# Performance work log

Measured on AMD Instinct MI355X. Metric: run time of the kernel, lower is better.

Reference implementation:

```python
import jax, jax.numpy as jnp
import numpy as np

EPS = 0.5


def setup_inputs() -> dict:
    key = jax.random.key(0)
    k_x, k_e, k_w1, k_b1, k_w2, k_b2 = jax.random.split(key, 6)
    N, E = 100000, 600000
    D_IN, D_HID, D_OUT = 128, 256, 128
    x = jax.random.normal(k_x, (N, D_IN), dtype=jnp.float32)
    edge_index = jax.random.randint(k_e, (2, E), 0, N, dtype=jnp.int64)
    # nn.Linear params: weight [out, in], bias [out]; kaiming-uniform-ish init
    lim1 = 1.0 / np.sqrt(D_IN)
    W1 = jax.random.uniform(k_w1, (D_HID, D_IN), minval=-lim1, maxval=lim1, dtype=jnp.float32)
    b1 = jax.random.uniform(k_b1, (D_HID,), minval=-lim1, maxval=lim1, dtype=jnp.float32)
    lim2 = 1.0 / np.sqrt(D_HID)
    W2 = jax.random.uniform(k_w2, (D_OUT, D_HID), minval=-lim2, maxval=lim2, dtype=jnp.float32)
    b2 = jax.random.uniform(k_b2, (D_OUT,), minval=-lim2, maxval=lim2, dtype=jnp.float32)
    return {"x": x, "edge_index": edge_index, "W1": W1, "b1": b1, "W2": W2, "b2": b2}


def reference(x, edge_index, W1, b1, W2, b2):
    # gather both endpoint features per edge and sum: [E, D_IN]
    s = x[edge_index[0]] + x[edge_index[1]]
    # 2-layer MLP: Linear -> ReLU -> Linear
    h = jax.nn.relu(s @ W1.T + b1)          # [E, D_HID]
    edge_attr = h @ W2.T + b2               # [E, D_OUT]
    return EPS * edge_attr
```

## Files before the change

kernel.cpp:

```cpp
#include <hip/hip_runtime.h>
#include <hip/hip_bf16.h>

#define EDGES 600000
#define DIN 128
#define DHID 256
#define DOUT 128

#define NCHUNK 37500
#define NBLK 256
#define THREADS 768
#define NWAVES 3072
#define STRIDE NWAVES

#define W2_OFF 65536
#define B1_OFF 131072
#define B2_OFF 132096
#define LDS_BYTES 132608

typedef __attribute__((ext_vector_type(4))) float floatx4;
typedef __attribute__((ext_vector_type(4))) short shortx4;
typedef __attribute__((ext_vector_type(8))) short shortx8;

__device__ inline unsigned short f2bf_rne(float f) {
    union { float f; unsigned u; } v; v.f = f;
    unsigned r = v.u + 0x7FFFu + ((v.u >> 16) & 1u);
    return (unsigned short)(r >> 16);
}

__global__ __launch_bounds__(256) void prep_kernel(
        const float* __restrict__ W1, const float* __restrict__ W2,
        unsigned short* __restrict__ ws) {
    int j = blockIdx.x * 256 + threadIdx.x;
    if (j < 4096) {
        int lane = j & 63, fs = j >> 6;
        int ks = fs & 3, t = fs >> 2;
        int hid = t * 16 + (lane & 15), q = lane >> 4;
        const float* src = W1 + hid * DIN + ks * 32 + q * 8;
        shortx8 v;
        #pragma unroll
        for (int i = 0; i < 8; ++i) v[i] = (short)f2bf_rne(src[i]);
        *((shortx8*)ws + j) = v;
    } else if (j < 12288) {
        int j2 = j - 4096;
        int lane = j2 & 63, fs = j2 >> 6;
        int ot = fs & 7, t = fs >> 3;
        int o = ot * 16 + (lane & 15), q = lane >> 4;
        const float* src = W2 + o * DHID + t * 16 + q * 4;
        shortx4 v;
        #pragma unroll
        for (int i = 0; i < 4; ++i) v[i] = (short)f2bf_rne(src[i]);
        *((shortx4*)(ws + 32768) + j2) = v;
    }
}

#define GATHER(RAW, NA, NB) do {                                              \
    const float* pa_ = x + (size_t)(NA) * DIN + q * 8;                        \
    const float* pb_ = x + (size_t)(NB) * DIN + q * 8;                        \
    _Pragma("unroll")                                                         \
    for (int ks_ = 0; ks_ < 4; ++ks_) {                                       \
        RAW[ks_*4+0] = *(const float4*)(pa_ + ks_*32);                        \
        RAW[ks_*4+1] = *(const float4*)(pa_ + ks_*32 + 4);                    \
        RAW[ks_*4+2] = *(const float4*)(pb_ + ks_*32);                        \
        RAW[ks_*4+3] = *(const float4*)(pb_ + ks_*32 + 4);                    \
    }                                                                         \
} while (0)

__global__ __launch_bounds__(THREADS, 3) void gin_kernel(
        const float* __restrict__ x, const int* __restrict__ ei,
        const float* __restrict__ b1, const float* __restrict__ b2,
        const unsigned short* __restrict__ wsw,
        float* __restrict__ out) {
    extern __shared__ char smem[];
    const int tid = threadIdx.x;
    const int lane = tid & 63, q = lane >> 4, col = lane & 15;

    const int gw = blockIdx.x * 12 + (tid >> 6);
    int ch = gw;
    const int e0 = ch * 16 + col;
    const int na0 = ei[e0];
    const int nb0 = ei[EDGES + e0];

    {
        const float4* gsrc = (const float4*)wsw;
        for (int idx = tid; idx < 8192; idx += THREADS) {
            float4 v = gsrc[idx];
            *(float4*)(smem + (size_t)idx * 16) = v;
        }
        if (tid < 384) {
            float v = (tid < 256) ? b1[tid] : b2[tid - 256];
            *(float*)(smem + B1_OFF + tid * 4) = v;
        }
    }

    float4 raw[16];
    GATHER(raw, na0, nb0);

    int naN, nbN;
    {
        const int e1 = (ch + STRIDE) * 16 + col;
        naN = ei[e1];
        nbN = ei[EDGES + e1];
    }
    __syncthreads();

    const shortx8* w1l = (const shortx8*)smem + lane;
    const shortx4* w2l = (const shortx4*)(smem + W2_OFF) + lane;
    const floatx4* b1l = (const floatx4*)(smem + B1_OFF) + q;
    const floatx4* b2l = (const floatx4*)(smem + B2_OFF) + q;

    for (;;) {
        shortx8 sfrag[4];
        #pragma unroll
        for (int ks = 0; ks < 4; ++ks) {
            float4 u0 = raw[ks*4+0], u1 = raw[ks*4+1];
            float4 v0 = raw[ks*4+2], v1 = raw[ks*4+3];
            union { shortx8 s8; __hip_bfloat162 b[4]; } pk;
            pk.b[0] = __float22bfloat162_rn(make_float2(u0.x+v0.x, u0.y+v0.y));
            pk.b[1] = __float22bfloat162_rn(make_float2(u0.z+v0.z, u0.w+v0.w));
            pk.b[2] = __float22bfloat162_rn(make_float2(u1.x+v1.x, u1.y+v1.y));
            pk.b[3] = __float22bfloat162_rn(make_float2(u1.z+v1.z, u1.w+v1.w));
            sfrag[ks] = pk.s8;
        }

        const int chN = ch + STRIDE;
        const bool haveN = (chN < NCHUNK);
        if (haveN) {
            GATHER(raw, naN, nbN);
            const int ch2 = chN + STRIDE;
            if (ch2 < NCHUNK) {
                const int e2 = ch2 * 16 + col;
                naN = ei[e2];
                nbN = ei[EDGES + e2];
            }
        }

        floatx4 acc2[8];
        #pragma unroll
        for (int ot = 0; ot < 8; ++ot) acc2[ot] = b2l[ot*4];

        #pragma unroll 1
        for (int t = 0; t < 16; ++t) {
            shortx8 a1[4];
            #pragma unroll
            for (int ks = 0; ks < 4; ++ks) a1[ks] = w1l[(t*4+ks)*64];
            floatx4 acc1 = b1l[t*4];
            #pragma unroll
            for (int ks = 0; ks < 4; ++ks)
                acc1 = __builtin_amdgcn_mfma_f32_16x16x32_bf16(a1[ks], sfrag[ks], acc1, 0, 0, 0);
            union { shortx4 s4; __hip_bfloat162 b[2]; } pk;
            pk.b[0] = __float22bfloat162_rn(make_float2(fmaxf(acc1[0], 0.f), fmaxf(acc1[1], 0.f)));
            pk.b[1] = __float22bfloat162_rn(make_float2(fmaxf(acc1[2], 0.f), fmaxf(acc1[3], 0.f)));
            const shortx4 hf = pk.s4;
            #pragma unroll
            for (int ot = 0; ot < 8; ++ot) {
                shortx4 wb = w2l[(t*8+ot)*64];
                acc2[ot] = __builtin_amdgcn_mfma_f32_16x16x16bf16_1k(wb, hf, acc2[ot], 0, 0, 0);
            }
        }

        {
            float* op = out + (size_t)(ch * 16 + col) * DOUT + q * 4;
            #pragma unroll
            for (int ot = 0; ot < 8; ++ot) {
                floatx4 v = acc2[ot] * 0.5f;
                __builtin_nontemporal_store(v, (floatx4*)(op + ot * 16));
            }
        }

        if (!haveN) break;
        ch = chN;
    }
}

extern "C" void kernel_launch(void* const* d_in, const int* in_sizes, int n_in,
                              void* d_out, int out_size, void* d_ws, size_t ws_size,
                              hipStream_t stream) {
    const float* x  = (const float*)d_in[0];
    const int*   ei = (const int*)d_in[1];
    const float* W1 = (const float*)d_in[2];
    const float* b1 = (const float*)d_in[3];
    const float* W2 = (const float*)d_in[4];
    const float* b2 = (const float*)d_in[5];
    unsigned short* ws = (unsigned short*)d_ws;

    static bool attr_done = false;
    if (!attr_done) {
        (void)hipFuncSetAttribute((const void*)gin_kernel,
                                  hipFuncAttributeMaxDynamicSharedMemorySize,
                                  LDS_BYTES);
        attr_done = true;
    }

    prep_kernel<<<48, 256, 0, stream>>>(W1, W2, ws);
    gin_kernel<<<NBLK, THREADS, LDS_BYTES, stream>>>(x, ei, b1, b2, ws, (float*)d_out);
}
```

Before: 470.5 us.

## Pre-convert node features to bf16 to halve gather traffic

Adds a prep kernel that converts x to bf16 in workspace, and the main kernel gathers bf16 rows instead of fp32, halving gather bytes and register footprint for the prefetch buffer. Sums are computed from bf16-rounded inputs, which adds a small extra rounding before the sum. Output stores switch from nontemporal to regular stores. A fallback fp32 path is kept when the workspace is too small.

```diff
diff --git a/kernel.cpp b/kernel.cpp
--- a/kernel.cpp
+++ b/kernel.cpp
@@ -5,17 +5,20 @@
 #define DIN 128
 #define DHID 256
 #define DOUT 128
+#define NNODES 100000
 
 #define NCHUNK 37500
 #define NBLK 256
 #define THREADS 768
-#define NWAVES 3072
-#define STRIDE NWAVES
+#define STRIDE 3072
 
 #define W2_OFF 65536
 #define B1_OFF 131072
 #define B2_OFF 132096
 #define LDS_BYTES 132608
+
+#define XB_OFF_SHORTS 65536
+#define WS_BYTES_NEEDED (131072ull + (unsigned long long)NNODES * DIN * 2ull)
 
 typedef __attribute__((ext_vector_type(4))) float floatx4;
 typedef __attribute__((ext_vector_type(4))) short shortx4;
@@ -53,20 +56,22 @@
     }
 }
 
-#define GATHER(RAW, NA, NB) do {                                              \
-    const float* pa_ = x + (size_t)(NA) * DIN + q * 8;                        \
-    const float* pb_ = x + (size_t)(NB) * DIN + q * 8;                        \
-    _Pragma("unroll")                                                         \
-    for (int ks_ = 0; ks_ < 4; ++ks_) {                                       \
-        RAW[ks_*4+0] = *(const float4*)(pa_ + ks_*32);                        \
-        RAW[ks_*4+1] = *(const float4*)(pa_ + ks_*32 + 4);                    \
-        RAW[ks_*4+2] = *(const float4*)(pb_ + ks_*32);                        \
-        RAW[ks_*4+3] = *(const float4*)(pb_ + ks_*32 + 4);                    \
-    }                                                                         \
-} while (0)
-
+__global__ __launch_bounds__(256) void prep_x(
+        const float* __restrict__ x, unsigned short* __restrict__ xb) {
+    const int total = NNODES * DIN / 4;
+    for (int i = blockIdx.x * 256 + threadIdx.x; i < total; i += gridDim.x * 256) {
+        float4 v = ((const float4*)x)[i];
+        shortx4 o;
+        o[0] = (short)f2bf_rne(v.x); o[1] = (short)f2bf_rne(v.y);
+        o[2] = (short)f2bf_rne(v.z); o[3] = (short)f2bf_rne(v.w);
+        *((shortx4*)xb + i) = o;
+    }
+}
+
+template <bool BFX>
 __global__ __launch_bounds__(THREADS, 3) void gin_kernel(
-        const float* __restrict__ x, const int* __restrict__ ei,
+        const float* __restrict__ x, const unsigned short* __restrict__ xb,
+        const int* __restrict__ ei,
         const float* __restrict__ b1, const float* __restrict__ b2,
         const unsigned short* __restrict__ wsw,
         float* __restrict__ out) {
@@ -76,6 +81,32 @@
 
     const int gw = blockIdx.x * 12 + (tid >> 6);
     int ch = gw;
+
+    float4  rawf[BFX ? 1 : 16];
+    shortx8 rawb[BFX ? 8 : 1];
+
+    auto gather = [&](int na, int nb) {
+        if constexpr (BFX) {
+            const shortx8* pa = (const shortx8*)xb + (size_t)na * 16 + q;
+            const shortx8* pb = (const shortx8*)xb + (size_t)nb * 16 + q;
+            #pragma unroll
+            for (int ks = 0; ks < 4; ++ks) {
+                rawb[ks*2+0] = pa[ks*4];
+                rawb[ks*2+1] = pb[ks*4];
+            }
+        } else {
+            const float* pa = x + (size_t)na * DIN + q * 8;
+            const float* pb = x + (size_t)nb * DIN + q * 8;
+            #pragma unroll
+            for (int ks = 0; ks < 4; ++ks) {
+                rawf[ks*4+0] = *(const float4*)(pa + ks*32);
+                rawf[ks*4+1] = *(const float4*)(pa + ks*32 + 4);
+                rawf[ks*4+2] = *(const float4*)(pb + ks*32);
+                rawf[ks*4+3] = *(const float4*)(pb + ks*32 + 4);
+            }
+        }
+    };
+
     const int e0 = ch * 16 + col;
     const int na0 = ei[e0];
     const int nb0 = ei[EDGES + e0];
@@ -92,8 +123,7 @@
         }
     }
 
-    float4 raw[16];
-    GATHER(raw, na0, nb0);
+    gather(na0, nb0);
 
     int naN, nbN;
     {
@@ -110,22 +140,37 @@
 
     for (;;) {
         shortx8 sfrag[4];
-        #pragma unroll
-        for (int ks = 0; ks < 4; ++ks) {
-            float4 u0 = raw[ks*4+0], u1 = raw[ks*4+1];
-            float4 v0 = raw[ks*4+2], v1 = raw[ks*4+3];
-            union { shortx8 s8; __hip_bfloat162 b[4]; } pk;
-            pk.b[0] = __float22bfloat162_rn(make_float2(u0.x+v0.x, u0.y+v0.y));
-            pk.b[1] = __float22bfloat162_rn(make_float2(u0.z+v0.z, u0.w+v0.w));
-            pk.b[2] = __float22bfloat162_rn(make_float2(u1.x+v1.x, u1.y+v1.y));
-            pk.b[3] = __float22bfloat162_rn(make_float2(u1.z+v1.z, u1.w+v1.w));
-            sfrag[ks] = pk.s8;
+        if constexpr (BFX) {
+            #pragma unroll
+            for (int ks = 0; ks < 4; ++ks) {
+                union { shortx8 s8; __hip_bfloat162 h[4]; } A, B, S;
+                A.s8 = rawb[ks*2]; B.s8 = rawb[ks*2+1];
+                #pragma unroll
+                for (int j = 0; j < 4; ++j) {
+                    float2 fa = __bfloat1622float2(A.h[j]);
+                    float2 fb = __bfloat1622float2(B.h[j]);
+                    S.h[j] = __float22bfloat162_rn(make_float2(fa.x + fb.x, fa.y + fb.y));
+                }
+                sfrag[ks] = S.s8;
+            }
+        } else {
+            #pragma unroll
+            for (int ks = 0; ks < 4; ++ks) {
+                float4 u0 = rawf[ks*4+0], u1 = rawf[ks*4+1];
+                float4 v0 = rawf[ks*4+2], v1 = rawf[ks*4+3];
+                union { shortx8 s8; __hip_bfloat162 b[4]; } pk;
+                pk.b[0] = __float22bfloat162_rn(make_float2(u0.x+v0.x, u0.y+v0.y));
+                pk.b[1] = __float22bfloat162_rn(make_float2(u0.z+v0.z, u0.w+v0.w));
+                pk.b[2] = __float22bfloat162_rn(make_float2(u1.x+v1.x, u1.y+v1.y));
+                pk.b[3] = __float22bfloat162_rn(make_float2(u1.z+v1.z, u1.w+v1.w));
+                sfrag[ks] = pk.s8;
+            }
         }
 
         const int chN = ch + STRIDE;
         const bool haveN = (chN < NCHUNK);
         if (haveN) {
-            GATHER(raw, naN, nbN);
+            gather(naN, nbN);
             const int ch2 = chN + STRIDE;
             if (ch2 < NCHUNK) {
                 const int e2 = ch2 * 16 + col;
@@ -163,7 +208,7 @@
             #pragma unroll
             for (int ot = 0; ot < 8; ++ot) {
                 floatx4 v = acc2[ot] * 0.5f;
-                __builtin_nontemporal_store(v, (floatx4*)(op + ot * 16));
+                *(floatx4*)(op + ot * 16) = v;
             }
         }
 
@@ -185,12 +230,23 @@
 
     static bool attr_done = false;
     if (!attr_done) {
-        (void)hipFuncSetAttribute((const void*)gin_kernel,
+        (void)hipFuncSetAttribute((const void*)gin_kernel<true>,
+                                  hipFuncAttributeMaxDynamicSharedMemorySize,
+                                  LDS_BYTES);
+        (void)hipFuncSetAttribute((const void*)gin_kernel<false>,
                                   hipFuncAttributeMaxDynamicSharedMemorySize,
                                   LDS_BYTES);
         attr_done = true;
     }
 
     prep_kernel<<<48, 256, 0, stream>>>(W1, W2, ws);
-    gin_kernel<<<NBLK, THREADS, LDS_BYTES, stream>>>(x, ei, b1, b2, ws, (float*)d_out);
-}
+    if (ws_size >= WS_BYTES_NEEDED) {
+        unsigned short* xb = ws + XB_OFF_SHORTS;
+        prep_x<<<2048, 256, 0, stream>>>(x, xb);
+        gin_kernel<true><<<NBLK, THREADS, LDS_BYTES, stream>>>(
+            x, xb, ei, b1, b2, ws, (float*)d_out);
+    } else {
+        gin_kernel<false><<<NBLK, THREADS, LDS_BYTES, stream>>>(
+            x, nullptr, ei, b1, b2, ws, (float*)d_out);
+    }
+}
```

New measurement: 435.8 us. 7.4% less time.
